# Performance work log

Hardware: AMD Instinct MI355X
Metric: run time of the kernel (lower is better)

Reference implementation:

```python
import jax, jax.numpy as jnp
from jax import lax
import numpy as np

V = 30000   # vocab_size
E = 64      # embedding_dim
H = 64      # lstm_units
K = 9       # num_tags
B = 512
T = 512


def setup_inputs() -> dict:
    key = jax.random.key(0)
    ks = jax.random.split(key, 12)
    s = 0.05
    return {
        "tokens": jax.random.randint(ks[0], (B, T), 0, V),
        "emb":   jax.random.normal(ks[1], (V + 1, E), dtype=jnp.float32) * s,
        "Wf": jax.random.normal(ks[2], (E, 4 * H), dtype=jnp.float32) * s,
        "Uf": jax.random.normal(ks[3], (H, 4 * H), dtype=jnp.float32) * s,
        "bf": jnp.zeros((4 * H,), dtype=jnp.float32),
        "Wb": jax.random.normal(ks[4], (E, 4 * H), dtype=jnp.float32) * s,
        "Ub": jax.random.normal(ks[5], (H, 4 * H), dtype=jnp.float32) * s,
        "bb": jnp.zeros((4 * H,), dtype=jnp.float32),
        "Wd": jax.random.normal(ks[6], (2 * H, K), dtype=jnp.float32) * s,
        "bd": jnp.zeros((K,), dtype=jnp.float32),
        "trans": jax.random.normal(ks[7], (K, K), dtype=jnp.float32) * s,
    }


def _lstm(x_tm, mask_tm, W, U, b):
    """Keras-convention LSTM over time-major x_tm [T,B,E]; masked steps carry state."""
    Bsz = x_tm.shape[1]
    h0 = jnp.zeros((Bsz, U.shape[0]), x_tm.dtype)
    c0 = jnp.zeros_like(h0)

    def step(carry, inp):
        h, c = carry
        xt, mt = inp                      # xt [B,E], mt [B] bool
        z = xt @ W + h @ U + b            # [B,4H], gate order i,f,g,o
        i, f, g, o = jnp.split(z, 4, axis=-1)
        c_new = jax.nn.sigmoid(f) * c + jax.nn.sigmoid(i) * jnp.tanh(g)
        h_new = jax.nn.sigmoid(o) * jnp.tanh(c_new)
        m = mt[:, None]
        h2 = jnp.where(m, h_new, h)
        c2 = jnp.where(m, c_new, c)
        return (h2, c2), h2

    _, hs = lax.scan(step, (h0, c0), (x_tm, mask_tm))
    return hs                              # [T,B,H]


def _viterbi(pot, mask, trans):
    """Batched Viterbi decode. pot [B,T,K], mask [B,T] bool, trans [K,K]."""
    pot_t = pot.transpose(1, 0, 2)         # [T,B,K]
    m_t = mask.T                           # [T,B]
    alpha0 = pot_t[0]
    ident = jnp.arange(K, dtype=jnp.int32)[None, :]

    def step(alpha, inp):
        p, m = inp                         # p [B,K], m [B]
        scores = alpha[:, :, None] + trans[None]   # [B, prev K, next K]
        best = scores.max(axis=1)
        bp = scores.argmax(axis=1).astype(jnp.int32)
        mm = m[:, None]
        alpha_new = jnp.where(mm, best + p, alpha)
        bp = jnp.where(mm, bp, ident)
        return alpha_new, bp

    alpha, bps = lax.scan(step, alpha0, (pot_t[1:], m_t[1:]))   # bps [T-1,B,K]
    last = alpha.argmax(axis=-1).astype(jnp.int32)              # [B]

    def back(tag, bp):
        prev = jnp.take_along_axis(bp, tag[:, None], axis=1)[:, 0]
        return prev, prev

    _, ys = lax.scan(back, last, bps, reverse=True)             # ys[t] = tag_t, t<T-1
    tags = jnp.concatenate([ys, last[None]], axis=0).T          # [B,T]
    return jnp.where(mask, tags, 0)


def reference(tokens, emb, Wf, Uf, bf, Wb, Ub, bb, Wd, bd, trans):
    mask = tokens != 0                     # mask_zero semantics
    x = emb[tokens]                        # [B,T,E]
    x_tm = x.transpose(1, 0, 2)            # [T,B,E]
    m_tm = mask.T
    hf = _lstm(x_tm, m_tm, Wf, Uf, bf)                     # forward dir
    hb = _lstm(x_tm[::-1], m_tm[::-1], Wb, Ub, bb)[::-1]   # backward dir
    h = jnp.concatenate([hf, hb], axis=-1).transpose(1, 0, 2)  # [B,T,2H]
    potentials = h @ Wd + bd               # CRF emission potentials [B,T,K]
    decoded = _viterbi(potentials, mask, trans)
    seq_len = mask.sum(axis=1).astype(jnp.int32)
    return decoded, potentials, seq_len
```

## Files before the change

### kernel.cpp

```cpp
#include <hip/hip_runtime.h>

#define BB 512
#define TT 512
#define KK 9
#define VP1 30001
#define BTK ((size_t)BB * TT * KK)

typedef __attribute__((ext_vector_type(8))) short short8;
typedef __attribute__((ext_vector_type(4))) float float4v;

__device__ __forceinline__ float sigm(float x) {
    return __builtin_amdgcn_rcpf(1.0f + __expf(-x));
}
__device__ __forceinline__ float tanh_(float x) {
    return 1.0f - 2.0f * __builtin_amdgcn_rcpf(__expf(2.0f * x) + 1.0f);
}

__device__ __forceinline__ unsigned short f2bf(float f) {
    unsigned int u = __float_as_uint(f);
    unsigned int r = u + 0x7fffu + ((u >> 16) & 1u);
    return (unsigned short)(r >> 16);
}
__device__ __forceinline__ float bflo2f(unsigned int d) { return __uint_as_float(d << 16); }
__device__ __forceinline__ float bfhi2f(unsigned int d) { return __uint_as_float(d & 0xffff0000u); }

__device__ __forceinline__ float bcast(float v, int i) {
    return __uint_as_float(__builtin_amdgcn_readlane(__float_as_uint(v), i));
}

__device__ __forceinline__ void block_sync_lds() {
    __builtin_amdgcn_s_waitcnt(0xC07F);
    __builtin_amdgcn_s_barrier();
}

__global__ __launch_bounds__(256)
void wswz_kernel(const float* __restrict__ Wf, const float* __restrict__ bfv,
                 const float* __restrict__ Wb, const float* __restrict__ bbv,
                 unsigned short* __restrict__ wswz, float* __restrict__ bsw)
{
    const int tid = threadIdx.x;
#pragma unroll
    for (int it = 0; it < 16; ++it) {
        int o = blockIdx.x * 4096 + it * 256 + tid;
        int k = o & 63, c = o >> 6;
        int dir = c >> 8, rem = c & 255;
        int u = rem >> 2, g = rem & 3;
        float val = (dir ? Wb : Wf)[k * 256 + g * 64 + u];
        wswz[o] = f2bf(val);
    }
    if (blockIdx.x == 0) {
#pragma unroll
        for (int h = 0; h < 2; ++h) {
            int c = h * 256 + tid;
            int dir = c >> 8, rem = c & 255;
            bsw[c] = (dir ? bbv : bfv)[(rem & 3) * 64 + (rem >> 2)];
        }
    }
}

__global__ __launch_bounds__(256, 1)
void embw_kernel(const float* __restrict__ emb,
                 const unsigned short* __restrict__ wswz, const float* __restrict__ bsw,
                 unsigned short* __restrict__ embw)
{
    const int v0 = blockIdx.x * 64;
    const int tid = threadIdx.x;
    const int w = tid >> 6, lane = tid & 63;
    const int l16 = lane & 15, quad = lane >> 4;

    __shared__ __align__(16) unsigned short clds[64][520];

    short8 bFr[8][2];
    float biasn[8];
#pragma unroll
    for (int n = 0; n < 8; ++n) {
        int c = w * 128 + n * 16 + l16;
        biasn[n] = bsw[c];
        const unsigned short* wp = wswz + c * 64;
#pragma unroll
        for (int q = 0; q < 2; ++q)
            bFr[n][q] = *(const short8*)(wp + q * 32 + quad * 8);
    }

    short8 aFr[4][2];
#pragma unroll
    for (int mt = 0; mt < 4; ++mt) {
        int vrow = v0 + mt * 16 + l16;
        if (vrow >= VP1) vrow = VP1 - 1;
        const float* er = emb + (size_t)vrow * 64;
#pragma unroll
        for (int q = 0; q < 2; ++q) {
            const float* p = er + q * 32 + quad * 8;
            float4 x0 = *(const float4*)(p);
            float4 x1 = *(const float4*)(p + 4);
            short8 v;
            v[0] = (short)f2bf(x0.x); v[1] = (short)f2bf(x0.y);
            v[2] = (short)f2bf(x0.z); v[3] = (short)f2bf(x0.w);
            v[4] = (short)f2bf(x1.x); v[5] = (short)f2bf(x1.y);
            v[6] = (short)f2bf(x1.z); v[7] = (short)f2bf(x1.w);
            aFr[mt][q] = v;
        }
    }

    float4v acc[4][8];
#pragma unroll
    for (int mt = 0; mt < 4; ++mt)
#pragma unroll
        for (int n = 0; n < 8; ++n) {
            acc[mt][n][0] = biasn[n]; acc[mt][n][1] = biasn[n];
            acc[mt][n][2] = biasn[n]; acc[mt][n][3] = biasn[n];
        }
#pragma unroll
    for (int mt = 0; mt < 4; ++mt)
#pragma unroll
        for (int n = 0; n < 8; ++n) {
            acc[mt][n] = __builtin_amdgcn_mfma_f32_16x16x32_bf16(aFr[mt][0], bFr[n][0], acc[mt][n], 0, 0, 0);
            acc[mt][n] = __builtin_amdgcn_mfma_f32_16x16x32_bf16(aFr[mt][1], bFr[n][1], acc[mt][n], 0, 0, 0);
        }

#pragma unroll
    for (int mt = 0; mt < 4; ++mt)
#pragma unroll
        for (int n = 0; n < 8; ++n) {
            int cc = w * 128 + n * 16 + l16;
#pragma unroll
            for (int r = 0; r < 4; ++r)
                clds[mt * 16 + quad * 4 + r][cc] = f2bf(acc[mt][n][r]);
        }
    __syncthreads();

#pragma unroll
    for (int it = 0; it < 16; ++it) {
        int idx = it * 256 + tid;
        int row = idx >> 6, chunk = idx & 63;
        if (v0 + row < VP1) {
            uint4 val = *(const uint4*)&clds[row][chunk * 8];
            *(uint4*)(embw + (size_t)(v0 + row) * 512 + chunk * 8) = val;
        }
    }
}

__global__ __launch_bounds__(256, 1)
void rec_kernel(const int* __restrict__ tokens,
                const unsigned short* __restrict__ embw,
                const float* __restrict__ Uf, const float* __restrict__ Ub,
                const float* __restrict__ Wd,
                float* __restrict__ potf, float* __restrict__ potb)
{
    const int blk = blockIdx.x;
    const int dir = blk >> 7;
    const int row0 = (blk & 127) * 4;
    const int tid = threadIdx.x;
    const int lane = tid & 63;
    const int w = tid >> 6;
    const int l16 = lane & 15, quad = lane >> 4;
    const int u = w * 16 + l16;

    const float* Up = dir ? Ub : Uf;
    float* pot = dir ? potb : potf;
    const uint2* ebase = (const uint2*)embw + dir * 64 + u;

    __shared__ int tokl[4][TT];
    __shared__ __align__(16) unsigned short hl[2][16][72];

    for (int i = tid; i < 2 * 16 * 72; i += 256)
        ((unsigned short*)hl)[i] = 0;
    for (int i = tid; i < 4 * TT; i += 256) {
        int r = i >> 9, t = i & 511;
        tokl[r][t] = tokens[(row0 + r) * TT + t];
    }

    short8 bU[4][2];
#pragma unroll
    for (int g = 0; g < 4; ++g)
#pragma unroll
        for (int q = 0; q < 2; ++q) {
            short8 v;
#pragma unroll
            for (int j = 0; j < 8; ++j) {
                int k = q * 32 + quad * 8 + j;
                v[j] = (short)f2bf(Up[k * 256 + g * 64 + u]);
            }
            bU[g][q] = v;
        }
    short8 bW[2];
#pragma unroll
    for (int q = 0; q < 2; ++q) {
        short8 v;
#pragma unroll
        for (int j = 0; j < 8; ++j) {
            int k = q * 32 + quad * 8 + j;
            v[j] = (l16 < KK) ? (short)f2bf(Wd[(dir * 64 + k) * KK + l16]) : (short)0;
        }
        bW[q] = v;
    }

    __syncthreads();

    int tokA[4], tokB[4];
    uint2 zxp[4];
#pragma unroll
    for (int d = 0; d < 4; ++d) {
        int td = dir ? (TT - 1 - d) : d;
        int td4 = dir ? (TT - 1 - (d + 4)) : (d + 4);
        tokA[d] = tokl[quad][td];
        tokB[d] = tokl[quad][td4];
    }
#pragma unroll
    for (int d = 0; d < 4; ++d)
        zxp[d] = ebase[(size_t)tokA[d] << 7];

    float c_st = 0.f, h_st = 0.f;

    float4v accg[4];
#pragma unroll
    for (int g = 0; g < 4; ++g) {
        accg[g][0] = 0.f; accg[g][1] = 0.f; accg[g][2] = 0.f; accg[g][3] = 0.f;
    }

    const int tprev0 = dir ? (w == 0 ? TT - 4 : TT - w) : (w == 0 ? 3 : w - 1);
    int vOff = (((row0 + quad) * TT + tprev0) * KK + l16) * 4;
    const int vStep = (dir ? -4 : 4) * KK * 4;

    for (int sb = 0; sb < TT; sb += 4) {
#pragma unroll
        for (int ss = 0; ss < 4; ++ss) {
            const int s = sb + ss;
            int tcur = tokA[ss];
            uint2 zcur = zxp[ss];

            hl[ss & 1][quad * 4][u] = f2bf(h_st);

            if (s + 4 < TT)
                zxp[ss] = ebase[(size_t)tokB[ss] << 7];
            tokA[ss] = tokB[ss];

            block_sync_lds();

            const unsigned short* hrow = &hl[ss & 1][l16][0];
            short8 a0 = *(const short8*)(hrow + quad * 8);
            short8 a1 = *(const short8*)(hrow + 32 + quad * 8);

            if (s + 8 < TT) {
                int t8 = dir ? (TT - 1 - (s + 8)) : (s + 8);
                tokB[ss] = tokl[quad][t8];
            }

            accg[0][0] = bflo2f(zcur.x);
            accg[1][0] = bfhi2f(zcur.x);
            accg[2][0] = bflo2f(zcur.y);
            accg[3][0] = bfhi2f(zcur.y);
#pragma unroll
            for (int g = 0; g < 4; ++g) {
                accg[g] = __builtin_amdgcn_mfma_f32_16x16x32_bf16(a0, bU[g][0], accg[g], 0, 0, 0);
                accg[g] = __builtin_amdgcn_mfma_f32_16x16x32_bf16(a1, bU[g][1], accg[g], 0, 0, 0);
            }

            if (w == ss && s > 0) {
                float4v accP = {0.f, 0.f, 0.f, 0.f};
                accP = __builtin_amdgcn_mfma_f32_16x16x32_bf16(a0, bW[0], accP, 0, 0, 0);
                accP = __builtin_amdgcn_mfma_f32_16x16x32_bf16(a1, bW[1], accP, 0, 0, 0);
                if (l16 < KK)
                    *(float*)((char*)pot + vOff) = accP[0];
                vOff += vStep;
            }

            {
                float zi = accg[0][0], zf = accg[1][0], zg = accg[2][0], zo = accg[3][0];
                float cn = sigm(zf) * c_st + sigm(zi) * tanh_(zg);
                float hn = sigm(zo) * tanh_(cn);
                bool m = (tcur != 0);
                h_st = m ? hn : h_st;
                c_st = m ? cn : c_st;
            }
        }
    }

    hl[0][quad * 4][u] = f2bf(h_st);
    block_sync_lds();
    if (w == 0) {
        const unsigned short* hrow = &hl[0][l16][0];
        short8 a0 = *(const short8*)(hrow + quad * 8);
        short8 a1 = *(const short8*)(hrow + 32 + quad * 8);
        float4v accP = {0.f, 0.f, 0.f, 0.f};
        accP = __builtin_amdgcn_mfma_f32_16x16x32_bf16(a0, bW[0], accP, 0, 0, 0);
        accP = __builtin_amdgcn_mfma_f32_16x16x32_bf16(a1, bW[1], accP, 0, 0, 0);
        int tlast = dir ? 0 : (TT - 1);
        if (l16 < KK)
            pot[((size_t)(row0 + quad) * TT + tlast) * KK + l16] = accP[0];
    }
}

__global__ __launch_bounds__(64)
void viterbi_kernel(const int* __restrict__ tokens,
                    const float* __restrict__ potf, const float* __restrict__ potb,
                    const float* __restrict__ bd, const float* __restrict__ trans,
                    float* __restrict__ dec_out, float* __restrict__ pot_out,
                    float* __restrict__ seq_out)
{
    const int row = blockIdx.x;
    const int lane = threadIdx.x;

    __shared__ float pl[TT * KK + 16];
    __shared__ unsigned char bpl[(TT - 1) * KK];
    __shared__ unsigned char maskl[TT + 8];
    __shared__ unsigned char segmap[64][KK];
    __shared__ unsigned char bseq[65];
    __shared__ float decl_[TT];
    __shared__ float bdl[16];

    if (lane < KK) bdl[lane] = bd[lane];
    if (lane < 8) maskl[TT + lane] = 0;
    pl[TT * KK + lane % 16] = 0.f;

    int cnt = 0;
#pragma unroll
    for (int ch = 0; ch < TT / 64; ++ch) {
        int tk = tokens[row * TT + ch * 64 + lane];
        int m = (tk != 0) ? 1 : 0;
        maskl[ch * 64 + lane] = (unsigned char)m;
        cnt += m;
    }
    for (int off = 32; off > 0; off >>= 1) cnt += __shfl_down(cnt, off);
    if (lane == 0) seq_out[row] = (float)cnt;

    const size_t base = (size_t)row * (TT * KK);
    int r9 = lane % KK;
    for (int i = 0; i < (TT * KK) / 64; ++i) {
        int li = i * 64 + lane;
        float s = potf[base + li] + potb[base + li] + bdl[r9];
        pl[li] = s;
        pot_out[base + li] = s;
        r9 = (r9 + 1 == KK) ? 0 : r9 + 1;
    }
    __syncthreads();

    float treg[KK];
#pragma unroll
    for (int i = 0; i < KK; ++i) treg[i] = (lane < KK) ? trans[i * KK + lane] : 0.f;

    float alpha = (lane < KK) ? pl[lane] : -1e30f;
    float pnext = (lane < KK) ? pl[KK + lane] : 0.f;
    int mnext = maskl[1];
#pragma unroll 4
    for (int t = 1; t < TT; ++t) {
        float p = pnext;
        int m = mnext;
        pnext = (lane < KK) ? pl[(t + 1) * KK + lane] : 0.f;
        mnext = maskl[t + 1];

        float sc[KK];
#pragma unroll
        for (int i = 0; i < KK; ++i) sc[i] = bcast(alpha, i) + treg[i];
        float b0 = fmaxf(fmaxf(fmaxf(sc[0], sc[1]), sc[2]),
                   fmaxf(fmaxf(fmaxf(sc[3], sc[4]), sc[5]),
                         fmaxf(fmaxf(sc[6], sc[7]), sc[8])));
        int i0 = 8;
#pragma unroll
        for (int i = 7; i >= 0; --i) i0 = (sc[i] == b0) ? i : i0;

        alpha = m ? (b0 + p) : alpha;
        int bpv = m ? i0 : lane;
        if (lane < KK) bpl[(t - 1) * KK + lane] = (unsigned char)bpv;
    }
    float sc[KK];
#pragma unroll
    for (int i = 0; i < KK; ++i) sc[i] = bcast(alpha, i);
    float b0 = fmaxf(fmaxf(fmaxf(sc[0], sc[1]), sc[2]),
               fmaxf(fmaxf(fmaxf(sc[3], sc[4]), sc[5]),
                     fmaxf(fmaxf(sc[6], sc[7]), sc[8])));
    int last = 8;
#pragma unroll
    for (int i = 7; i >= 0; --i) last = (sc[i] == b0) ? i : last;
    __syncthreads();

    {
        int l = lane;
#pragma unroll
        for (int x = 0; x < KK; ++x) {
            int y = x;
#pragma unroll
            for (int d = 7; d >= 0; --d) {
                int t = 8 * l + d;
                if (t < TT - 1) y = bpl[t * KK + y];
            }
            segmap[l][x] = (unsigned char)y;
        }
    }
    __syncthreads();
    if (lane == 0) {
        int cur = last;
        bseq[64] = (unsigned char)last;
        for (int l = 63; l >= 0; --l) {
            cur = segmap[l][cur];
            bseq[l] = (unsigned char)cur;
        }
    }
    __syncthreads();
    {
        int l = lane;
        int cur = bseq[l + 1];
#pragma unroll
        for (int d = 7; d >= 0; --d) {
            int t = 8 * l + d;
            if (t < TT - 1) cur = bpl[t * KK + cur];
            decl_[t] = (maskl[t] != 0) ? (float)cur : 0.f;
        }
    }
    __syncthreads();
#pragma unroll
    for (int ch = 0; ch < TT / 64; ++ch)
        dec_out[(size_t)row * TT + ch * 64 + lane] = decl_[ch * 64 + lane];
}

extern "C" void kernel_launch(void* const* d_in, const int* in_sizes, int n_in,
                              void* d_out, int out_size, void* d_ws, size_t ws_size,
                              hipStream_t stream)
{
    const int*   tokens = (const int*)d_in[0];
    const float* emb    = (const float*)d_in[1];
    const float* Wf     = (const float*)d_in[2];
    const float* Uf     = (const float*)d_in[3];
    const float* bfv    = (const float*)d_in[4];
    const float* Wb     = (const float*)d_in[5];
    const float* Ub     = (const float*)d_in[6];
    const float* bbv    = (const float*)d_in[7];
    const float* Wd     = (const float*)d_in[8];
    const float* bd     = (const float*)d_in[9];
    const float* trans  = (const float*)d_in[10];

    float* out     = (float*)d_out;
    float* dec_out = out;
    float* pot_out = out + (size_t)BB * TT;
    float* seq_out = out + (size_t)BB * TT + BTK;

    float* potf = (float*)d_ws;
    float* potb = potf + BTK;
    unsigned short* embw = (unsigned short*)(potb + BTK);
    unsigned short* wswz = (unsigned short*)potf;
    float* bsw = (float*)((char*)potf + 512 * 64 * sizeof(unsigned short));

    hipLaunchKernelGGL(wswz_kernel, dim3(8), dim3(256), 0, stream,
                       Wf, bfv, Wb, bbv, wswz, bsw);
    hipLaunchKernelGGL(embw_kernel, dim3(469), dim3(256), 0, stream,
                       emb, wswz, bsw, embw);
    hipLaunchKernelGGL(rec_kernel, dim3(256), dim3(256), 0, stream,
                       tokens, embw, Uf, Ub, Wd, potf, potb);
    hipLaunchKernelGGL(viterbi_kernel, dim3(BB), dim3(64), 0, stream,
                       tokens, potf, potb, bd, trans, dec_out, pot_out, seq_out);
}
```

Measured before the change: 398.1 us.

## Split recurrence into one row per block and stream potentials in Viterbi

The LSTM recurrence kernel now assigns one batch row per block and launches 1024 blocks instead of packing four rows into each block's MFMA tiles. The quads now compute the same row redundantly, and only quad 0 writes potentials. The intent is to let several independent latency-bound recurrence chains share each CU, trading the free four-row packing for more concurrent waves. The Viterbi kernel drops its LDS staging of potentials and instead keeps an 8-deep register ring of forward and backward potentials, prefetched from global memory during the loop.

```diff
diff --git a/kernel.cpp b/kernel.cpp
--- a/kernel.cpp
+++ b/kernel.cpp
@@ -148,8 +148,8 @@
                 float* __restrict__ potf, float* __restrict__ potb)
 {
     const int blk = blockIdx.x;
-    const int dir = blk >> 7;
-    const int row0 = (blk & 127) * 4;
+    const int dir = blk >> 9;
+    const int row = blk & 511;
     const int tid = threadIdx.x;
     const int lane = tid & 63;
     const int w = tid >> 6;
@@ -160,15 +160,13 @@
     float* pot = dir ? potb : potf;
     const uint2* ebase = (const uint2*)embw + dir * 64 + u;
 
-    __shared__ int tokl[4][TT];
+    __shared__ int tokl[TT];
     __shared__ __align__(16) unsigned short hl[2][16][72];
 
     for (int i = tid; i < 2 * 16 * 72; i += 256)
         ((unsigned short*)hl)[i] = 0;
-    for (int i = tid; i < 4 * TT; i += 256) {
-        int r = i >> 9, t = i & 511;
-        tokl[r][t] = tokens[(row0 + r) * TT + t];
-    }
+    for (int i = tid; i < TT; i += 256)
+        tokl[i] = tokens[row * TT + i];
 
     short8 bU[4][2];
 #pragma unroll
@@ -203,8 +201,8 @@
     for (int d = 0; d < 4; ++d) {
         int td = dir ? (TT - 1 - d) : d;
         int td4 = dir ? (TT - 1 - (d + 4)) : (d + 4);
-        tokA[d] = tokl[quad][td];
-        tokB[d] = tokl[quad][td4];
+        tokA[d] = tokl[td];
+        tokB[d] = tokl[td4];
     }
 #pragma unroll
     for (int d = 0; d < 4; ++d)
@@ -219,7 +217,7 @@
     }
 
     const int tprev0 = dir ? (w == 0 ? TT - 4 : TT - w) : (w == 0 ? 3 : w - 1);
-    int vOff = (((row0 + quad) * TT + tprev0) * KK + l16) * 4;
+    int vOff = ((row * TT + tprev0) * KK + l16) * 4;
     const int vStep = (dir ? -4 : 4) * KK * 4;
 
     for (int sb = 0; sb < TT; sb += 4) {
@@ -243,7 +241,7 @@
 
             if (s + 8 < TT) {
                 int t8 = dir ? (TT - 1 - (s + 8)) : (s + 8);
-                tokB[ss] = tokl[quad][t8];
+                tokB[ss] = tokl[t8];
             }
 
             accg[0][0] = bflo2f(zcur.x);
@@ -260,7 +258,7 @@
                 float4v accP = {0.f, 0.f, 0.f, 0.f};
                 accP = __builtin_amdgcn_mfma_f32_16x16x32_bf16(a0, bW[0], accP, 0, 0, 0);
                 accP = __builtin_amdgcn_mfma_f32_16x16x32_bf16(a1, bW[1], accP, 0, 0, 0);
-                if (l16 < KK)
+                if (quad == 0 && l16 < KK)
                     *(float*)((char*)pot + vOff) = accP[0];
                 vOff += vStep;
             }
@@ -286,8 +284,8 @@
         accP = __builtin_amdgcn_mfma_f32_16x16x32_bf16(a0, bW[0], accP, 0, 0, 0);
         accP = __builtin_amdgcn_mfma_f32_16x16x32_bf16(a1, bW[1], accP, 0, 0, 0);
         int tlast = dir ? 0 : (TT - 1);
-        if (l16 < KK)
-            pot[((size_t)(row0 + quad) * TT + tlast) * KK + l16] = accP[0];
+        if (quad == 0 && l16 < KK)
+            pot[((size_t)row * TT + tlast) * KK + l16] = accP[0];
     }
 }
 
@@ -301,17 +299,13 @@
     const int row = blockIdx.x;
     const int lane = threadIdx.x;
 
-    __shared__ float pl[TT * KK + 16];
     __shared__ unsigned char bpl[(TT - 1) * KK];
     __shared__ unsigned char maskl[TT + 8];
     __shared__ unsigned char segmap[64][KK];
     __shared__ unsigned char bseq[65];
     __shared__ float decl_[TT];
-    __shared__ float bdl[16];
-
-    if (lane < KK) bdl[lane] = bd[lane];
+
     if (lane < 8) maskl[TT + lane] = 0;
-    pl[TT * KK + lane % 16] = 0.f;
 
     int cnt = 0;
 #pragma unroll
@@ -325,29 +319,46 @@
     if (lane == 0) seq_out[row] = (float)cnt;
 
     const size_t base = (size_t)row * (TT * KK);
-    int r9 = lane % KK;
-    for (int i = 0; i < (TT * KK) / 64; ++i) {
-        int li = i * 64 + lane;
-        float s = potf[base + li] + potb[base + li] + bdl[r9];
-        pl[li] = s;
-        pot_out[base + li] = s;
-        r9 = (r9 + 1 == KK) ? 0 : r9 + 1;
-    }
-    __syncthreads();
+    const float* pfr = potf + base;
+    const float* pbr = potb + base;
+    const float bdv = (lane < KK) ? bd[lane] : 0.f;
+
+    {
+        int r9 = lane % KK;
+        for (int i = 0; i < (TT * KK) / 64; ++i) {
+            int li = i * 64 + lane;
+            float bdl = bcast(bdv, r9);
+            pot_out[base + li] = pfr[li] + pbr[li] + bdl;
+            r9 = (r9 + 1 == KK) ? 0 : r9 + 1;
+        }
+    }
 
     float treg[KK];
 #pragma unroll
     for (int i = 0; i < KK; ++i) treg[i] = (lane < KK) ? trans[i * KK + lane] : 0.f;
 
-    float alpha = (lane < KK) ? pl[lane] : -1e30f;
-    float pnext = (lane < KK) ? pl[KK + lane] : 0.f;
+    float alpha = (lane < KK) ? (pfr[lane] + pbr[lane] + bdv) : -1e30f;
+
+    float pfR[8], pbR[8];
+#pragma unroll
+    for (int d = 0; d < 8; ++d) {
+        int idx = (1 + d) * KK + lane;
+        pfR[d] = (lane < KK) ? pfr[idx] : 0.f;
+        pbR[d] = (lane < KK) ? pbr[idx] : 0.f;
+    }
     int mnext = maskl[1];
-#pragma unroll 4
+
+#pragma unroll 8
     for (int t = 1; t < TT; ++t) {
-        float p = pnext;
+        const int d = (t - 1) & 7;
+        float p = pfR[d] + pbR[d] + bdv;
         int m = mnext;
-        pnext = (lane < KK) ? pl[(t + 1) * KK + lane] : 0.f;
         mnext = maskl[t + 1];
+        if (t + 8 < TT) {
+            int idx = (t + 8) * KK + lane;
+            pfR[d] = (lane < KK) ? pfr[idx] : 0.f;
+            pbR[d] = (lane < KK) ? pbr[idx] : 0.f;
+        }
 
         float sc[KK];
 #pragma unroll
@@ -444,7 +455,7 @@
                        Wf, bfv, Wb, bbv, wswz, bsw);
     hipLaunchKernelGGL(embw_kernel, dim3(469), dim3(256), 0, stream,
                        emb, wswz, bsw, embw);
-    hipLaunchKernelGGL(rec_kernel, dim3(256), dim3(256), 0, stream,
+    hipLaunchKernelGGL(rec_kernel, dim3(1024), dim3(256), 0, stream,
                        tokens, embw, Uf, Ub, Wd, potf, potb);
     hipLaunchKernelGGL(viterbi_kernel, dim3(BB), dim3(64), 0, stream,
                        tokens, potf, potb, bd, trans, dec_out, pot_out, seq_out);
```

After: 726.0 us. +82.4%, slower.
